# Kernel tuning notes

Measured on AMD Instinct MI355X. Metric: run time of the kernel, lower is better.

The kernel has to match this reference:

```python
import jax, jax.numpy as jnp
import numpy as np

N = 100000
E = 1600000

def _norms(src, dst):
    ones = jnp.ones(src.shape[0], dtype=jnp.float32)
    out_deg = jax.ops.segment_sum(ones, src, num_segments=N)
    in_deg = jax.ops.segment_sum(ones, dst, num_segments=N)
    # dgl clamps degree to >=1; with self-loops deg>=1 anyway
    out_norm = jax.lax.rsqrt(jnp.clip(out_deg, 1.0))
    in_norm = jax.lax.rsqrt(jnp.clip(in_deg, 1.0))
    return out_norm, in_norm

def _graph_conv(x, W, b, src, dst, out_norm, in_norm):
    h = (x * out_norm[:, None]) @ W          # [N, dout]
    msg = h[src]                              # gather  [E', dout]
    agg = jax.ops.segment_sum(msg, dst, num_segments=N)
    return agg * in_norm[:, None] + b

def setup_inputs() -> dict:
    key = jax.random.key(0)
    ks = jax.random.split(key, 8)
    feat = jax.random.normal(ks[0], (N, 128), dtype=jnp.float32)
    src = jax.random.randint(ks[1], (E,), 0, N, dtype=jnp.int32)
    dst = jax.random.randint(ks[2], (E,), 0, N, dtype=jnp.int32)
    s1 = 1.0 / np.sqrt(128.0)
    W1 = jax.random.uniform(ks[3], (128, 128), jnp.float32, -s1, s1)
    b1 = jnp.zeros((128,), jnp.float32)
    W2 = jax.random.uniform(ks[4], (128, 128), jnp.float32, -s1, s1)
    b2 = jnp.zeros((128,), jnp.float32)
    W3 = jax.random.uniform(ks[5], (128, 64), jnp.float32, -s1, s1)
    b3 = jnp.zeros((64,), jnp.float32)
    return {"feat": feat, "src": src, "dst": dst,
            "W1": W1, "b1": b1, "W2": W2, "b2": b2, "W3": W3, "b3": b3}

def reference(feat, src, dst, W1, b1, W2, b2, W3, b3):
    # dgl.add_self_loop
    loop = jnp.arange(N, dtype=src.dtype)
    s = jnp.concatenate([src, loop])
    d = jnp.concatenate([dst, loop])
    out_norm, in_norm = _norms(s, d)
    # dropout is identity in eval mode (deterministic reference)
    h = jax.nn.relu(_graph_conv(feat, W1, b1, s, d, out_norm, in_norm))
    h = jax.nn.relu(_graph_conv(h, W2, b2, s, d, out_norm, in_norm))
    h = _graph_conv(h, W3, b3, s, d, out_norm, in_norm)
    return h
```

## Files before the change

### kernel.cpp

```cpp
#include <hip/hip_runtime.h>
#include <hip/hip_fp16.h>


#define NFEAT 128
#define BBITS 8
#define BSZ 256
#define EPB 4096

union H8 { float4 f4; __half2 h2[4]; };

using half8v = __attribute__((ext_vector_type(8))) _Float16;
using f32x4  = __attribute__((ext_vector_type(4))) float;

__global__ __launch_bounds__(256) void hist_kernel(const int* __restrict__ src,
                                                   const int* __restrict__ dst,
                                                   int* __restrict__ histD,
                                                   int* __restrict__ histS,
                                                   int NB, int nblk, int E) {
    __shared__ int hd[512], hs[512];
    const int t = threadIdx.x, b = blockIdx.x;
    for (int u = t; u < 512; u += 256) { hd[u] = 0; hs[u] = 0; }
    __syncthreads();
    const int base4 = b * (EPB / 4);
    #pragma unroll
    for (int j = 0; j < 4; ++j) {
        int i4 = base4 + j * 256 + t;
        int e0 = i4 * 4;
        if (e0 + 3 < E) {
            int4 s = ((const int4*)src)[i4];
            int4 d = ((const int4*)dst)[i4];
            atomicAdd(&hs[s.x >> BBITS], 1); atomicAdd(&hs[s.y >> BBITS], 1);
            atomicAdd(&hs[s.z >> BBITS], 1); atomicAdd(&hs[s.w >> BBITS], 1);
            atomicAdd(&hd[d.x >> BBITS], 1); atomicAdd(&hd[d.y >> BBITS], 1);
            atomicAdd(&hd[d.z >> BBITS], 1); atomicAdd(&hd[d.w >> BBITS], 1);
        } else {
            for (int e = e0; e < E && e < e0 + 4; ++e) {
                atomicAdd(&hs[src[e] >> BBITS], 1);
                atomicAdd(&hd[dst[e] >> BBITS], 1);
            }
        }
    }
    __syncthreads();
    for (int u = t; u < NB; u += 256) {
        histD[u * nblk + b] = hd[u];
        histS[u * nblk + b] = hs[u];
    }
}

__global__ __launch_bounds__(256) void scan1_kernel(const int* __restrict__ cnt,
                                                    int* __restrict__ excl,
                                                    int* __restrict__ blk_sum, int n) {
    const int tid = threadIdx.x, lane = tid & 63, wid = tid >> 6;
    const int i = blockIdx.x * 256 + tid;
    int v = (i < n) ? cnt[i] : 0;
    int incl = v;
    #pragma unroll
    for (int off = 1; off < 64; off <<= 1) {
        int t = __shfl_up(incl, off, 64);
        if (lane >= off) incl += t;
    }
    __shared__ int ws[4];
    if (lane == 63) ws[wid] = incl;
    __syncthreads();
    int woff = 0;
    #pragma unroll
    for (int w = 0; w < 3; ++w) if (w < wid) woff += ws[w];
    if (i < n) excl[i] = woff + incl - v;
    if (tid == 0) blk_sum[blockIdx.x] = ws[0] + ws[1] + ws[2] + ws[3];
}

__global__ __launch_bounds__(1024) void scan2_kernel(int* __restrict__ blk,
                                                     int* __restrict__ grand_total, int nb) {
    const int tid = threadIdx.x, lane = tid & 63, wid = tid >> 6;
    int v = (tid < nb) ? blk[tid] : 0;
    int incl = v;
    #pragma unroll
    for (int off = 1; off < 64; off <<= 1) {
        int t = __shfl_up(incl, off, 64);
        if (lane >= off) incl += t;
    }
    __shared__ int ws[16];
    if (lane == 63) ws[wid] = incl;
    __syncthreads();
    int woff = 0;
    #pragma unroll
    for (int w = 0; w < 15; ++w) if (w < wid) woff += ws[w];
    int excl = woff + incl - v;
    if (tid < nb) blk[tid] = excl;
    if (tid == nb - 1) *grand_total = excl + v;
}

__global__ void scan3_kernel(int* __restrict__ excl, const int* __restrict__ blk, int n) {
    int i = blockIdx.x * 256 + threadIdx.x;
    if (i < n) excl[i] += blk[blockIdx.x];
}

__global__ __launch_bounds__(256) void scatter_kernel(const int* __restrict__ src,
                                                      const int* __restrict__ dst,
                                                      const int* __restrict__ offD,
                                                      const int* __restrict__ offS,
                                                      int* __restrict__ bsrc,
                                                      int* __restrict__ bdst,
                                                      int* __restrict__ ssrc,
                                                      int NB, int nblk, int E) {
    __shared__ int hd[512], hs[512], baseD[512], baseS[512];
    const int t = threadIdx.x, b = blockIdx.x;
    for (int u = t; u < 512; u += 256) { hd[u] = 0; hs[u] = 0; }
    for (int u = t; u < NB; u += 256) {
        baseD[u] = offD[u * nblk + b];
        baseS[u] = offS[u * nblk + b];
    }
    __syncthreads();
    const int base4 = b * (EPB / 4);
    #pragma unroll
    for (int j = 0; j < 4; ++j) {
        int i4 = base4 + j * 256 + t;
        int e0 = i4 * 4;
        if (e0 + 3 < E) {
            int4 s = ((const int4*)src)[i4];
            int4 d = ((const int4*)dst)[i4];
            int se[4] = {s.x, s.y, s.z, s.w};
            int de[4] = {d.x, d.y, d.z, d.w};
            #pragma unroll
            for (int q = 0; q < 4; ++q) {
                int kd = de[q] >> BBITS;
                int pos = baseD[kd] + atomicAdd(&hd[kd], 1);
                bdst[pos] = de[q];
                bsrc[pos] = se[q];
                int ks = se[q] >> BBITS;
                int posS = baseS[ks] + atomicAdd(&hs[ks], 1);
                ssrc[posS] = se[q];
            }
        } else {
            for (int e = e0; e < E && e < e0 + 4; ++e) {
                int sv = src[e], dv = dst[e];
                int kd = dv >> BBITS;
                int pos = baseD[kd] + atomicAdd(&hd[kd], 1);
                bdst[pos] = dv;
                bsrc[pos] = sv;
                int ks = sv >> BBITS;
                int posS = baseS[ks] + atomicAdd(&hs[ks], 1);
                ssrc[posS] = sv;
            }
        }
    }
}

__global__ __launch_bounds__(256) void bucket_kernel(const int* __restrict__ bsrc,
                                                     const int* __restrict__ bdst,
                                                     const int* __restrict__ ssrc,
                                                     const int* __restrict__ offD,
                                                     const int* __restrict__ offS,
                                                     int* __restrict__ row_ptr,
                                                     int* __restrict__ col_idx,
                                                     float* __restrict__ in_norm,
                                                     float* __restrict__ out_norm,
                                                     int N, int NB, int nblk, int E) {
    __shared__ int cnt[BSZ], scnt[BSZ], start[BSZ], off[BSZ];
    __shared__ int ws[4];
    const int k = blockIdx.x, t = threadIdx.x;
    const int node0 = k << BBITS;
    cnt[t] = 0; scnt[t] = 0; off[t] = 0;
    __syncthreads();
    const int bB = offD[k * nblk], bE = (k + 1 < NB) ? offD[(k + 1) * nblk] : E;
    const int sB = offS[k * nblk], sE = (k + 1 < NB) ? offS[(k + 1) * nblk] : E;
    for (int i = bB + t; i < bE; i += 256) atomicAdd(&cnt[bdst[i] - node0], 1);
    for (int i = sB + t; i < sE; i += 256) atomicAdd(&scnt[ssrc[i] - node0], 1);
    __syncthreads();
    const int lane = t & 63, wid = t >> 6;
    int v = cnt[t];
    int incl = v;
    #pragma unroll
    for (int o = 1; o < 64; o <<= 1) {
        int x = __shfl_up(incl, o, 64);
        if (lane >= o) incl += x;
    }
    if (lane == 63) ws[wid] = incl;
    __syncthreads();
    int woff = 0;
    #pragma unroll
    for (int w = 0; w < 3; ++w) if (w < wid) woff += ws[w];
    start[t] = woff + incl - v;
    {
        int node = node0 + t;
        if (node < N) {
            row_ptr[node] = bB + start[t];
            in_norm[node]  = rsqrtf((float)(v + 1));
            out_norm[node] = rsqrtf((float)(scnt[t] + 1));
        }
    }
    if (k == 0 && t == 0) row_ptr[N] = E;
    __syncthreads();
    for (int i = bB + t; i < bE; i += 256) {
        int local = bdst[i] - node0;
        int r = atomicAdd(&off[local], 1);
        col_idx[bB + start[local] + r] = bsrc[i];
    }
}

__global__ void wt_kernel(const float* __restrict__ W, __half* __restrict__ Wt, int Ncols) {
    int n = blockIdx.x;
    int k = threadIdx.x;
    Wt[n * 128 + k] = __float2half(W[k * Ncols + n]);
}

template <int BN, typename XT>
__global__ __launch_bounds__(256) void mfma_gemm_kernel(const XT* __restrict__ x,
                                                        const __half* __restrict__ Wt,
                                                        const float* __restrict__ out_norm,
                                                        __half* __restrict__ h, int n_rows) {
    constexpr int BM = 64;
    constexpr int NT = BN / 16;
    __shared__ __half As[BM][136];
    __shared__ __half Bs[BN][136];
    const int tid  = threadIdx.x;
    const int row0 = blockIdx.x * BM;

    {
        int r  = tid >> 2;
        int c0 = (tid & 3) * 32;
        int grow = row0 + r;
        if (grow < n_rows) {
            float norm = out_norm[grow];
            if constexpr (sizeof(XT) == 4) {
                const float* xp = (const float*)x + (size_t)grow * NFEAT + c0;
                #pragma unroll
                for (int j = 0; j < 4; ++j) {
                    float4 p0 = *(const float4*)(xp + j * 8);
                    float4 p1 = *(const float4*)(xp + j * 8 + 4);
                    H8 u;
                    u.h2[0] = __floats2half2_rn(p0.x * norm, p0.y * norm);
                    u.h2[1] = __floats2half2_rn(p0.z * norm, p0.w * norm);
                    u.h2[2] = __floats2half2_rn(p1.x * norm, p1.y * norm);
                    u.h2[3] = __floats2half2_rn(p1.z * norm, p1.w * norm);
                    *(float4*)&As[r][c0 + j * 8] = u.f4;
                }
            } else {
                const __half* xp = (const __half*)x + (size_t)grow * NFEAT + c0;
                #pragma unroll
                for (int j = 0; j < 4; ++j) {
                    H8 u; u.f4 = *(const float4*)(xp + j * 8);
                    #pragma unroll
                    for (int q = 0; q < 4; ++q) {
                        float2 p = __half22float2(u.h2[q]);
                        u.h2[q] = __floats2half2_rn(p.x * norm, p.y * norm);
                    }
                    *(float4*)&As[r][c0 + j * 8] = u.f4;
                }
            }
        } else {
            H8 z; z.f4 = make_float4(0.f, 0.f, 0.f, 0.f);
            #pragma unroll
            for (int j = 0; j < 4; ++j) *(float4*)&As[r][c0 + j * 8] = z.f4;
        }
    }
    {
        constexpr int TPR = 256 / BN;
        constexpr int CH  = 128 / TPR;
        int wr = tid / TPR;
        int wc = (tid % TPR) * CH;
        const __half* wp = Wt + wr * 128 + wc;
        #pragma unroll
        for (int j = 0; j < CH / 8; ++j)
            *(float4*)&Bs[wr][wc + j * 8] = *(const float4*)(wp + j * 8);
    }
    __syncthreads();

    const int lane = tid & 63, wid = tid >> 6;
    const int lr = lane & 15, quad = lane >> 4;
    const int koff = quad * 8;
    f32x4 acc[NT];
    #pragma unroll
    for (int t = 0; t < NT; ++t) acc[t] = (f32x4){0.f, 0.f, 0.f, 0.f};

    #pragma unroll
    for (int ks = 0; ks < 4; ++ks) {
        half8v a = *(const half8v*)&As[wid * 16 + lr][ks * 32 + koff];
        #pragma unroll
        for (int nt = 0; nt < NT; ++nt) {
            half8v b = *(const half8v*)&Bs[nt * 16 + lr][ks * 32 + koff];
            acc[nt] = __builtin_amdgcn_mfma_f32_16x16x32_f16(a, b, acc[nt], 0, 0, 0);
        }
    }

    #pragma unroll
    for (int nt = 0; nt < NT; ++nt) {
        #pragma unroll
        for (int r = 0; r < 4; ++r) {
            int row = row0 + wid * 16 + quad * 4 + r;
            if (row < n_rows)
                h[(size_t)row * BN + nt * 16 + lr] = __float2half(acc[nt][r]);
        }
    }
}

template <int DOUT, bool RELU, typename OutT>
__global__ __launch_bounds__(256) void agg_kernel(const __half* __restrict__ h,
                                                  const int* __restrict__ row_ptr,
                                                  const int* __restrict__ col_idx,
                                                  const float* __restrict__ in_norm,
                                                  const float* __restrict__ bias,
                                                  OutT* __restrict__ out, int n) {
    constexpr int TPN = DOUT / 8;
    constexpr int NPB = 256 / TPN;
    const int tid  = threadIdx.x;
    const int sub  = tid / TPN;
    const int c    = (tid % TPN) * 8;
    const int node = blockIdx.x * NPB + sub;
    if (node >= n) return;

    float acc[8];
    {
        H8 u; u.f4 = *(const float4*)(h + (size_t)node * DOUT + c);
        #pragma unroll
        for (int q = 0; q < 4; ++q) {
            float2 p = __half22float2(u.h2[q]);
            acc[q * 2] = p.x; acc[q * 2 + 1] = p.y;
        }
    }
    int e  = row_ptr[node];
    int e1 = row_ptr[node + 1];
    for (; e + 3 < e1; e += 4) {
        int s0 = col_idx[e], s1 = col_idx[e + 1], s2 = col_idx[e + 2], s3 = col_idx[e + 3];
        H8 u0, u1, u2, u3;
        u0.f4 = *(const float4*)(h + (size_t)s0 * DOUT + c);
        u1.f4 = *(const float4*)(h + (size_t)s1 * DOUT + c);
        u2.f4 = *(const float4*)(h + (size_t)s2 * DOUT + c);
        u3.f4 = *(const float4*)(h + (size_t)s3 * DOUT + c);
        #pragma unroll
        for (int q = 0; q < 4; ++q) {
            float2 p0 = __half22float2(u0.h2[q]);
            float2 p1 = __half22float2(u1.h2[q]);
            float2 p2 = __half22float2(u2.h2[q]);
            float2 p3 = __half22float2(u3.h2[q]);
            acc[q * 2]     += (p0.x + p1.x) + (p2.x + p3.x);
            acc[q * 2 + 1] += (p0.y + p1.y) + (p2.y + p3.y);
        }
    }
    for (; e < e1; ++e) {
        int s0 = col_idx[e];
        H8 u0; u0.f4 = *(const float4*)(h + (size_t)s0 * DOUT + c);
        #pragma unroll
        for (int q = 0; q < 4; ++q) {
            float2 p0 = __half22float2(u0.h2[q]);
            acc[q * 2] += p0.x; acc[q * 2 + 1] += p0.y;
        }
    }
    float inn = in_norm[node];
    float r[8];
    #pragma unroll
    for (int q = 0; q < 8; ++q) {
        r[q] = acc[q] * inn + bias[c + q];
        if (RELU) r[q] = fmaxf(r[q], 0.0f);
    }
    if constexpr (sizeof(OutT) == 2) {
        H8 o;
        #pragma unroll
        for (int q = 0; q < 4; ++q) o.h2[q] = __floats2half2_rn(r[q * 2], r[q * 2 + 1]);
        *(float4*)((__half*)out + (size_t)node * DOUT + c) = o.f4;
    } else {
        float4 o0, o1;
        o0.x=r[0]; o0.y=r[1]; o0.z=r[2]; o0.w=r[3];
        o1.x=r[4]; o1.y=r[5]; o1.z=r[6]; o1.w=r[7];
        *(float4*)((float*)out + (size_t)node * DOUT + c)     = o0;
        *(float4*)((float*)out + (size_t)node * DOUT + c + 4) = o1;
    }
}

extern "C" void kernel_launch(void* const* d_in, const int* in_sizes, int n_in,
                              void* d_out, int out_size, void* d_ws, size_t ws_size,
                              hipStream_t stream) {
    const float* feat = (const float*)d_in[0];
    const int*   src  = (const int*)d_in[1];
    const int*   dst  = (const int*)d_in[2];
    const float* W1   = (const float*)d_in[3];
    const float* b1   = (const float*)d_in[4];
    const float* W2   = (const float*)d_in[5];
    const float* b2   = (const float*)d_in[6];
    const float* W3   = (const float*)d_in[7];
    const float* b3   = (const float*)d_in[8];

    const int N = in_sizes[0] / NFEAT;
    const int E = in_sizes[1];

    const int NB   = (N + BSZ - 1) / BSZ;
    const int nblk = (E + EPB - 1) / EPB;
    const int nh   = NB * nblk;
    const int nsb  = (nh + 255) / 256;

    char* ws = (char*)d_ws;
    auto alloc = [&](size_t bytes) {
        char* p = ws;
        ws += (bytes + 255) & ~(size_t)255;
        return p;
    };
    float* out_norm = (float*)alloc((size_t)N * 4);
    float* in_norm  = (float*)alloc((size_t)N * 4);
    int*   row_ptr  = (int*)alloc((size_t)(N + 1) * 4);
    int*   histD    = (int*)alloc((size_t)nh * 4);
    int*   histS    = (int*)alloc((size_t)nh * 4);
    int*   blk_sum  = (int*)alloc((size_t)1024 * 4);
    int*   scratch  = (int*)alloc((size_t)16 * 4);
    __half* Wt1     = (__half*)alloc((size_t)128 * 128 * 2);
    __half* Wt2     = (__half*)alloc((size_t)128 * 128 * 2);
    __half* Wt3     = (__half*)alloc((size_t)64 * 128 * 2);
    int*   col_idx  = (int*)alloc((size_t)E * 4);
    __half* hA      = (__half*)alloc((size_t)N * NFEAT * 2);
    __half* hB      = (__half*)alloc((size_t)N * NFEAT * 2);
    int*   bdst     = (int*)hA;
    int*   bsrc     = (int*)hA + E;
    int*   ssrc     = (int*)hA + 2 * (size_t)E;

    wt_kernel<<<128, 128, 0, stream>>>(W1, Wt1, 128);
    wt_kernel<<<128, 128, 0, stream>>>(W2, Wt2, 128);
    wt_kernel<<<64, 128, 0, stream>>>(W3, Wt3, 64);

    hist_kernel<<<nblk, 256, 0, stream>>>(src, dst, histD, histS, NB, nblk, E);
    scan1_kernel<<<nsb, 256, 0, stream>>>(histD, histD, blk_sum, nh);
    scan2_kernel<<<1, 1024, 0, stream>>>(blk_sum, scratch, nsb);
    scan3_kernel<<<nsb, 256, 0, stream>>>(histD, blk_sum, nh);
    scan1_kernel<<<nsb, 256, 0, stream>>>(histS, histS, blk_sum, nh);
    scan2_kernel<<<1, 1024, 0, stream>>>(blk_sum, scratch, nsb);
    scan3_kernel<<<nsb, 256, 0, stream>>>(histS, blk_sum, nh);
    scatter_kernel<<<nblk, 256, 0, stream>>>(src, dst, histD, histS, bsrc, bdst, ssrc, NB, nblk, E);
    bucket_kernel<<<NB, 256, 0, stream>>>(bsrc, bdst, ssrc, histD, histS, row_ptr, col_idx,
                                          in_norm, out_norm, N, NB, nblk, E);

    const int gb = (N + 63) / 64;
    mfma_gemm_kernel<128, float><<<gb, 256, 0, stream>>>(feat, Wt1, out_norm, hA, N);
    agg_kernel<128, true, __half><<<(N + 15) / 16, 256, 0, stream>>>(hA, row_ptr, col_idx,
                                                                     in_norm, b1, hB, N);
    mfma_gemm_kernel<128, __half><<<gb, 256, 0, stream>>>(hB, Wt2, out_norm, hA, N);
    agg_kernel<128, true, __half><<<(N + 15) / 16, 256, 0, stream>>>(hA, row_ptr, col_idx,
                                                                     in_norm, b2, hB, N);
    mfma_gemm_kernel<64, __half><<<gb, 256, 0, stream>>>(hB, Wt3, out_norm, hA, N);
    agg_kernel<64, false, float><<<(N + 31) / 32, 256, 0, stream>>>(hA, row_ptr, col_idx,
                                                                    in_norm, b3, (float*)d_out, N);
}
```

Before: 388.0 us.

## Pack bucketed edge data, merge histogram scans, and fuse weight transposes

The dst and src histograms now sit in one concatenated array, so a single scan sequence covers both. Each scan thread handles two elements, which cuts the launches from six scan kernels to three. The scatter stage now writes a packed 32-bit word holding the dst-local index and the src, plus a one-byte src-local index, instead of three int arrays, which reduces memory traffic in the scatter and bucket kernels. The three weight-transpose launches are merged into one. The packing assumes node ids fit in 24 bits and bucket size 256.

After: 357.2 us. 8.0% less time.

```diff
diff --git a/kernel.cpp b/kernel.cpp
--- a/kernel.cpp
+++ b/kernel.cpp
@@ -14,9 +14,8 @@
 
 __global__ __launch_bounds__(256) void hist_kernel(const int* __restrict__ src,
                                                    const int* __restrict__ dst,
-                                                   int* __restrict__ histD,
-                                                   int* __restrict__ histS,
-                                                   int NB, int nblk, int E) {
+                                                   int* __restrict__ hist2,
+                                                   int NB, int nblk, int nh, int E) {
     __shared__ int hd[512], hs[512];
     const int t = threadIdx.x, b = blockIdx.x;
     for (int u = t; u < 512; u += 256) { hd[u] = 0; hs[u] = 0; }
@@ -42,73 +41,75 @@
     }
     __syncthreads();
     for (int u = t; u < NB; u += 256) {
-        histD[u * nblk + b] = hd[u];
-        histS[u * nblk + b] = hs[u];
-    }
-}
-
-__global__ __launch_bounds__(256) void scan1_kernel(const int* __restrict__ cnt,
-                                                    int* __restrict__ excl,
+        hist2[u * nblk + b]      = hd[u];
+        hist2[nh + u * nblk + b] = hs[u];
+    }
+}
+
+__global__ __launch_bounds__(256) void scan1_kernel(int* __restrict__ data,
                                                     int* __restrict__ blk_sum, int n) {
     const int tid = threadIdx.x, lane = tid & 63, wid = tid >> 6;
-    const int i = blockIdx.x * 256 + tid;
-    int v = (i < n) ? cnt[i] : 0;
+    const int i2 = blockIdx.x * 256 + tid;
+    int a = 0, b = 0;
+    if (2 * i2 + 1 < n)      { int2 v = ((const int2*)data)[i2]; a = v.x; b = v.y; }
+    else if (2 * i2 < n)     { a = data[2 * i2]; }
+    int s = a + b;
+    int incl = s;
+    #pragma unroll
+    for (int off = 1; off < 64; off <<= 1) {
+        int t2 = __shfl_up(incl, off, 64);
+        if (lane >= off) incl += t2;
+    }
+    __shared__ int ws[4];
+    if (lane == 63) ws[wid] = incl;
+    __syncthreads();
+    int woff = 0;
+    #pragma unroll
+    for (int w = 0; w < 3; ++w) if (w < wid) woff += ws[w];
+    int pref = woff + incl - s;
+    if (2 * i2 < n)     data[2 * i2]     = pref;
+    if (2 * i2 + 1 < n) data[2 * i2 + 1] = pref + a;
+    if (tid == 0) blk_sum[blockIdx.x] = ws[0] + ws[1] + ws[2] + ws[3];
+}
+
+__global__ __launch_bounds__(1024) void scan2_kernel(int* __restrict__ blk, int nb) {
+    const int tid = threadIdx.x, lane = tid & 63, wid = tid >> 6;
+    int v = (tid < nb) ? blk[tid] : 0;
     int incl = v;
     #pragma unroll
     for (int off = 1; off < 64; off <<= 1) {
         int t = __shfl_up(incl, off, 64);
         if (lane >= off) incl += t;
     }
-    __shared__ int ws[4];
-    if (lane == 63) ws[wid] = incl;
-    __syncthreads();
-    int woff = 0;
-    #pragma unroll
-    for (int w = 0; w < 3; ++w) if (w < wid) woff += ws[w];
-    if (i < n) excl[i] = woff + incl - v;
-    if (tid == 0) blk_sum[blockIdx.x] = ws[0] + ws[1] + ws[2] + ws[3];
-}
-
-__global__ __launch_bounds__(1024) void scan2_kernel(int* __restrict__ blk,
-                                                     int* __restrict__ grand_total, int nb) {
-    const int tid = threadIdx.x, lane = tid & 63, wid = tid >> 6;
-    int v = (tid < nb) ? blk[tid] : 0;
-    int incl = v;
-    #pragma unroll
-    for (int off = 1; off < 64; off <<= 1) {
-        int t = __shfl_up(incl, off, 64);
-        if (lane >= off) incl += t;
-    }
     __shared__ int ws[16];
     if (lane == 63) ws[wid] = incl;
     __syncthreads();
     int woff = 0;
     #pragma unroll
     for (int w = 0; w < 15; ++w) if (w < wid) woff += ws[w];
-    int excl = woff + incl - v;
-    if (tid < nb) blk[tid] = excl;
-    if (tid == nb - 1) *grand_total = excl + v;
-}
-
-__global__ void scan3_kernel(int* __restrict__ excl, const int* __restrict__ blk, int n) {
-    int i = blockIdx.x * 256 + threadIdx.x;
-    if (i < n) excl[i] += blk[blockIdx.x];
+    if (tid < nb) blk[tid] = woff + incl - v;
+}
+
+__global__ __launch_bounds__(256) void scan3_kernel(int* __restrict__ data,
+                                                    const int* __restrict__ blk, int n) {
+    const int i2 = blockIdx.x * 256 + threadIdx.x;
+    int add = blk[blockIdx.x];
+    if (2 * i2 < n)     data[2 * i2]     += add;
+    if (2 * i2 + 1 < n) data[2 * i2 + 1] += add;
 }
 
 __global__ __launch_bounds__(256) void scatter_kernel(const int* __restrict__ src,
                                                       const int* __restrict__ dst,
-                                                      const int* __restrict__ offD,
-                                                      const int* __restrict__ offS,
-                                                      int* __restrict__ bsrc,
-                                                      int* __restrict__ bdst,
-                                                      int* __restrict__ ssrc,
-                                                      int NB, int nblk, int E) {
+                                                      const int* __restrict__ hist2,
+                                                      unsigned int* __restrict__ dstP,
+                                                      unsigned char* __restrict__ srcB,
+                                                      int NB, int nblk, int nh, int E) {
     __shared__ int hd[512], hs[512], baseD[512], baseS[512];
     const int t = threadIdx.x, b = blockIdx.x;
     for (int u = t; u < 512; u += 256) { hd[u] = 0; hs[u] = 0; }
     for (int u = t; u < NB; u += 256) {
-        baseD[u] = offD[u * nblk + b];
-        baseS[u] = offS[u * nblk + b];
+        baseD[u] = hist2[u * nblk + b];
+        baseS[u] = hist2[nh + u * nblk + b] - E;
     }
     __syncthreads();
     const int base4 = b * (EPB / 4);
@@ -125,47 +126,45 @@
             for (int q = 0; q < 4; ++q) {
                 int kd = de[q] >> BBITS;
                 int pos = baseD[kd] + atomicAdd(&hd[kd], 1);
-                bdst[pos] = de[q];
-                bsrc[pos] = se[q];
+                dstP[pos] = ((unsigned int)(de[q] & (BSZ - 1)) << 24) | (unsigned int)se[q];
                 int ks = se[q] >> BBITS;
                 int posS = baseS[ks] + atomicAdd(&hs[ks], 1);
-                ssrc[posS] = se[q];
+                srcB[posS] = (unsigned char)(se[q] & (BSZ - 1));
             }
         } else {
             for (int e = e0; e < E && e < e0 + 4; ++e) {
                 int sv = src[e], dv = dst[e];
                 int kd = dv >> BBITS;
                 int pos = baseD[kd] + atomicAdd(&hd[kd], 1);
-                bdst[pos] = dv;
-                bsrc[pos] = sv;
+                dstP[pos] = ((unsigned int)(dv & (BSZ - 1)) << 24) | (unsigned int)sv;
                 int ks = sv >> BBITS;
                 int posS = baseS[ks] + atomicAdd(&hs[ks], 1);
-                ssrc[posS] = sv;
+                srcB[posS] = (unsigned char)(sv & (BSZ - 1));
             }
         }
     }
 }
 
-__global__ __launch_bounds__(256) void bucket_kernel(const int* __restrict__ bsrc,
-                                                     const int* __restrict__ bdst,
-                                                     const int* __restrict__ ssrc,
-                                                     const int* __restrict__ offD,
-                                                     const int* __restrict__ offS,
+__global__ __launch_bounds__(256) void bucket_kernel(const unsigned int* __restrict__ dstP,
+                                                     const unsigned char* __restrict__ srcB,
+                                                     const int* __restrict__ hist2,
                                                      int* __restrict__ row_ptr,
                                                      int* __restrict__ col_idx,
                                                      float* __restrict__ in_norm,
                                                      float* __restrict__ out_norm,
-                                                     int N, int NB, int nblk, int E) {
+                                                     int N, int NB, int nblk, int nh, int E) {
     __shared__ int cnt[BSZ], scnt[BSZ], start[BSZ], off[BSZ];
     __shared__ int ws[4];
     const int k = blockIdx.x, t = threadIdx.x;
     const int node0 = k << BBITS;
     cnt[t] = 0; scnt[t] = 0; off[t] = 0;
     __syncthreads();
-    const int bB = offD[k * nblk], bE = (k + 1 < NB) ? offD[(k + 1) * nblk] : E;
-    const int sB = offS[k * nblk], sE = (k + 1 < NB) ? offS[(k + 1) * nblk] : E;
-    for (int i = bB + t; i < bE; i += 256) atomicAdd(&cnt[bdst[i] - node0], 1);
-    for (int i = sB + t; i < sE; i += 256) atomicAdd(&scnt[ssrc[i] - node0], 1);
+    const int bB = hist2[k * nblk];
+    const int bE = (k + 1 < NB) ? hist2[(k + 1) * nblk] : E;
+    const int sB = hist2[nh + k * nblk] - E;
+    const int sE = ((k + 1 < NB) ? hist2[nh + (k + 1) * nblk] : 2 * E) - E;
+    for (int i = bB + t; i < bE; i += 256) atomicAdd(&cnt[dstP[i] >> 24], 1);
+    for (int i = sB + t; i < sE; i += 256) atomicAdd(&scnt[srcB[i]], 1);
     __syncthreads();
     const int lane = t & 63, wid = t >> 6;
     int v = cnt[t];
@@ -192,16 +191,20 @@
     if (k == 0 && t == 0) row_ptr[N] = E;
     __syncthreads();
     for (int i = bB + t; i < bE; i += 256) {
-        int local = bdst[i] - node0;
+        unsigned int pv = dstP[i];
+        int local = pv >> 24;
         int r = atomicAdd(&off[local], 1);
-        col_idx[bB + start[local] + r] = bsrc[i];
-    }
-}
-
-__global__ void wt_kernel(const float* __restrict__ W, __half* __restrict__ Wt, int Ncols) {
-    int n = blockIdx.x;
-    int k = threadIdx.x;
-    Wt[n * 128 + k] = __float2half(W[k * Ncols + n]);
+        col_idx[bB + start[local] + r] = (int)(pv & 0xFFFFFFu);
+    }
+}
+
+__global__ void wt_all_kernel(const float* __restrict__ W1, const float* __restrict__ W2,
+                              const float* __restrict__ W3, __half* __restrict__ Wt1,
+                              __half* __restrict__ Wt2, __half* __restrict__ Wt3) {
+    int b = blockIdx.x, k = threadIdx.x;
+    if (b < 128)      Wt1[b * 128 + k] = __float2half(W1[k * 128 + b]);
+    else if (b < 256) { int n = b - 128; Wt2[n * 128 + k] = __float2half(W2[k * 128 + n]); }
+    else              { int n = b - 256; Wt3[n * 128 + k] = __float2half(W3[k * 64 + n]); }
 }
 
 template <int BN, typename XT>
@@ -386,7 +389,8 @@
     const int NB   = (N + BSZ - 1) / BSZ;
     const int nblk = (E + EPB - 1) / EPB;
     const int nh   = NB * nblk;
-    const int nsb  = (nh + 255) / 256;
+    const int n2   = 2 * nh;
+    const int nsb  = (n2 + 511) / 512;
 
     char* ws = (char*)d_ws;
     auto alloc = [&](size_t bytes) {
@@ -397,34 +401,26 @@
     float* out_norm = (float*)alloc((size_t)N * 4);
     float* in_norm  = (float*)alloc((size_t)N * 4);
     int*   row_ptr  = (int*)alloc((size_t)(N + 1) * 4);
-    int*   histD    = (int*)alloc((size_t)nh * 4);
-    int*   histS    = (int*)alloc((size_t)nh * 4);
+    int*   hist2    = (int*)alloc((size_t)n2 * 4);
     int*   blk_sum  = (int*)alloc((size_t)1024 * 4);
-    int*   scratch  = (int*)alloc((size_t)16 * 4);
     __half* Wt1     = (__half*)alloc((size_t)128 * 128 * 2);
     __half* Wt2     = (__half*)alloc((size_t)128 * 128 * 2);
     __half* Wt3     = (__half*)alloc((size_t)64 * 128 * 2);
     int*   col_idx  = (int*)alloc((size_t)E * 4);
     __half* hA      = (__half*)alloc((size_t)N * NFEAT * 2);
     __half* hB      = (__half*)alloc((size_t)N * NFEAT * 2);
-    int*   bdst     = (int*)hA;
-    int*   bsrc     = (int*)hA + E;
-    int*   ssrc     = (int*)hA + 2 * (size_t)E;
-
-    wt_kernel<<<128, 128, 0, stream>>>(W1, Wt1, 128);
-    wt_kernel<<<128, 128, 0, stream>>>(W2, Wt2, 128);
-    wt_kernel<<<64, 128, 0, stream>>>(W3, Wt3, 64);
-
-    hist_kernel<<<nblk, 256, 0, stream>>>(src, dst, histD, histS, NB, nblk, E);
-    scan1_kernel<<<nsb, 256, 0, stream>>>(histD, histD, blk_sum, nh);
-    scan2_kernel<<<1, 1024, 0, stream>>>(blk_sum, scratch, nsb);
-    scan3_kernel<<<nsb, 256, 0, stream>>>(histD, blk_sum, nh);
-    scan1_kernel<<<nsb, 256, 0, stream>>>(histS, histS, blk_sum, nh);
-    scan2_kernel<<<1, 1024, 0, stream>>>(blk_sum, scratch, nsb);
-    scan3_kernel<<<nsb, 256, 0, stream>>>(histS, blk_sum, nh);
-    scatter_kernel<<<nblk, 256, 0, stream>>>(src, dst, histD, histS, bsrc, bdst, ssrc, NB, nblk, E);
-    bucket_kernel<<<NB, 256, 0, stream>>>(bsrc, bdst, ssrc, histD, histS, row_ptr, col_idx,
-                                          in_norm, out_norm, N, NB, nblk, E);
+    unsigned int*  dstP = (unsigned int*)hA;
+    unsigned char* srcB = (unsigned char*)(dstP + E);
+
+    wt_all_kernel<<<320, 128, 0, stream>>>(W1, W2, W3, Wt1, Wt2, Wt3);
+
+    hist_kernel<<<nblk, 256, 0, stream>>>(src, dst, hist2, NB, nblk, nh, E);
+    scan1_kernel<<<nsb, 256, 0, stream>>>(hist2, blk_sum, n2);
+    scan2_kernel<<<1, 1024, 0, stream>>>(blk_sum, nsb);
+    scan3_kernel<<<nsb, 256, 0, stream>>>(hist2, blk_sum, n2);
+    scatter_kernel<<<nblk, 256, 0, stream>>>(src, dst, hist2, dstP, srcB, NB, nblk, nh, E);
+    bucket_kernel<<<NB, 256, 0, stream>>>(dstP, srcB, hist2, row_ptr, col_idx,
+                                          in_norm, out_norm, N, NB, nblk, nh, E);
 
     const int gb = (N + 63) / 64;
     mfma_gemm_kernel<128, float><<<gb, 256, 0, stream>>>(feat, Wt1, out_norm, hA, N);
```
